# Optimization experiments

Hardware: AMD Instinct MI355X
Metric: run time of the kernel (lower is better)

Reference implementation:

```python
import jax, jax.numpy as jnp
import numpy as np

B, S, D = 4, 2048, 1024
H = 16
DH = D // H  # head dim = 64
LN_EPS = 1e-5


def setup_inputs() -> dict:
    key = jax.random.key(0)
    ks = jax.random.split(key, 4)
    scale = 1.0 / np.sqrt(D)
    return {
        "hidden_states": jax.random.normal(ks[0], (B, S, D), dtype=jnp.float32),
        "ln_gamma": jnp.ones((D,), jnp.float32),
        "ln_beta": jnp.zeros((D,), jnp.float32),
        "Wq": jax.random.normal(ks[1], (D, D), dtype=jnp.float32) * scale,
        "bq": jnp.zeros((D,), jnp.float32),
        "Wk": jax.random.normal(ks[2], (D, D), dtype=jnp.float32) * scale,
        "bk": jnp.zeros((D,), jnp.float32),
        "Wv": jax.random.normal(ks[3], (D, D), dtype=jnp.float32) * scale,
        "bv": jnp.zeros((D,), jnp.float32),
    }


def _layernorm(x, gamma, beta):
    mu = jnp.mean(x, axis=-1, keepdims=True)
    var = jnp.mean(jnp.square(x - mu), axis=-1, keepdims=True)
    return (x - mu) * jax.lax.rsqrt(var + LN_EPS) * gamma + beta


def reference(hidden_states, ln_gamma, ln_beta, Wq, bq, Wk, bk, Wv, bv):
    x = _layernorm(hidden_states, ln_gamma, ln_beta)  # [B,S,D]
    # Linear uses y = x @ W.T + b (torch convention)
    q = x @ Wq.T + bq
    k = x @ Wk.T + bk
    v = x @ Wv.T + bv
    # split heads -> [B,H,S,DH]
    q = q.reshape(B, S, H, DH).transpose(0, 2, 1, 3)
    k = k.reshape(B, S, H, DH).transpose(0, 2, 1, 3)
    v = v.reshape(B, S, H, DH).transpose(0, 2, 1, 3)
    scores = jnp.einsum("bhsd,bhtd->bhst", q, k) / jnp.sqrt(jnp.float32(DH))
    probs = jax.nn.softmax(scores, axis=-1)
    ctx = jnp.einsum("bhst,bhtd->bhsd", probs, v)  # [B,H,S,DH]
    ctx = ctx.transpose(0, 2, 1, 3).reshape(B, S, H * DH)
    return ctx
```

## Files before the change

kernel.cpp:

```cpp
#include <hip/hip_runtime.h>

#define B_ 4
#define S_ 2048
#define D_ 1024
#define H_ 16
#define DH_ 64
#define M_ (B_*S_)
#define N_ (3*D_)
#define K_ D_

using f32x4 = __attribute__((ext_vector_type(4))) float;
using s16x8 = __attribute__((ext_vector_type(8))) short;
typedef unsigned short u16;
typedef unsigned int u32;

__device__ __forceinline__ u16 f2bf(float f) {
  u32 u = __float_as_uint(f);
  return (u16)((u + 0x7FFFu + ((u >> 16) & 1u)) >> 16);
}

__device__ __forceinline__ u32 cvt_pk_bf16(float lo, float hi) {
  u32 r;
  asm("v_cvt_pk_bf16_f32 %0, %1, %2" : "=v"(r) : "v"(lo), "v"(hi));
  return r;
}

__device__ __forceinline__ float hw_exp2(float x) {
#if __has_builtin(__builtin_amdgcn_exp2f)
  return __builtin_amdgcn_exp2f(x);
#else
  return exp2f(x);
#endif
}

__device__ __forceinline__ void pswap32(u32& a, u32& b) {
#if __has_builtin(__builtin_amdgcn_permlane32_swap)
  auto r = __builtin_amdgcn_permlane32_swap(a, b, false, false);
  a = r[0]; b = r[1];
#else
  asm volatile("v_permlane32_swap_b32 %0, %1" : "+v"(a), "+v"(b));
#endif
}
__device__ __forceinline__ void pswap16(u32& a, u32& b) {
#if __has_builtin(__builtin_amdgcn_permlane16_swap)
  auto r = __builtin_amdgcn_permlane16_swap(a, b, false, false);
  a = r[0]; b = r[1];
#else
  asm volatile("v_permlane16_swap_b32 %0, %1" : "+v"(a), "+v"(b));
#endif
}

__device__ __forceinline__ void gload16(const void* g, void* l) {
  __builtin_amdgcn_global_load_lds((const __attribute__((address_space(1))) u32*)g,
                                   (__attribute__((address_space(3))) u32*)l,
                                   16, 0, 0);
}

__global__ __launch_bounds__(256) void k_lnw(const float* __restrict__ hs,
                                             const float* __restrict__ gam,
                                             const float* __restrict__ bet,
                                             const float* __restrict__ wq,
                                             const float* __restrict__ wk,
                                             const float* __restrict__ wv,
                                             u16* __restrict__ xln,
                                             u16* __restrict__ wcat) {
  __shared__ float ps[4], ps2[4];
  int tid = threadIdx.x;
  if (blockIdx.x < M_) {
    int row = blockIdx.x;
    const float4* src = (const float4*)(hs + (size_t)row * D_);
    float4 x = src[tid];
    float s = x.x + x.y + x.z + x.w;
    float s2 = x.x * x.x + x.y * x.y + x.z * x.z + x.w * x.w;
#pragma unroll
    for (int m = 32; m >= 1; m >>= 1) {
      s += __shfl_xor(s, m, 64);
      s2 += __shfl_xor(s2, m, 64);
    }
    int w = tid >> 6, lane = tid & 63;
    if (lane == 0) { ps[w] = s; ps2[w] = s2; }
    __syncthreads();
    s = ps[0] + ps[1] + ps[2] + ps[3];
    s2 = ps2[0] + ps2[1] + ps2[2] + ps2[3];
    float mean = s * (1.0f / D_);
    float var = s2 * (1.0f / D_) - mean * mean;
    float inv = 1.0f / sqrtf(var + 1e-5f);
    float4 g4 = ((const float4*)gam)[tid];
    float4 b4 = ((const float4*)bet)[tid];
    ushort4 o;
    o.x = f2bf((x.x - mean) * inv * g4.x + b4.x);
    o.y = f2bf((x.y - mean) * inv * g4.y + b4.y);
    o.z = f2bf((x.z - mean) * inv * g4.z + b4.z);
    o.w = f2bf((x.w - mean) * inv * g4.w + b4.w);
    *(ushort4*)(xln + (size_t)row * D_ + tid * 4) = o;
  } else {
    int idx = (blockIdx.x - M_) * 256 + tid;
    int seg = idx >> 18;
    int off = idx & 262143;
    const float* src = (seg == 0) ? wq : (seg == 1) ? wk : wv;
    float4 x = ((const float4*)src)[off];
    ushort4 o;
    o.x = f2bf(x.x); o.y = f2bf(x.y); o.z = f2bf(x.z); o.w = f2bf(x.w);
    ((ushort4*)wcat)[idx] = o;
  }
}

#define BM 256
#define BN 128
#define BK 64
__global__ __launch_bounds__(512, 4) void k_qkv(const u16* __restrict__ xln,
                                                const u16* __restrict__ wcat,
                                                const float* __restrict__ bq,
                                                const float* __restrict__ bk,
                                                const float* __restrict__ bv,
                                                u16* __restrict__ qh,
                                                u16* __restrict__ kh,
                                                u16* __restrict__ vt) {
  __shared__ char smem[49152];
  char* smA = smem;
  char* smB = smem + BM * BK * 2;
  int blk = (blockIdx.x & 7) * 96 + (blockIdx.x >> 3);
  int bm = blk / (N_ / BN);
  int bn = blk % (N_ / BN);
  int tid = threadIdx.x;
  int lane = tid & 63, wid = tid >> 6;
  int wm = wid >> 1, wn = wid & 1;
  int lo = lane & 15, hi = lane >> 4;
  int mBase = bm * BM, nBase = bn * BN;

  f32x4 acc[4][4];
  f32x4 zero = {0.f, 0.f, 0.f, 0.f};
#pragma unroll
  for (int i = 0; i < 4; ++i)
#pragma unroll
    for (int j = 0; j < 4; ++j) acc[i][j] = zero;

  for (int kt = 0; kt < K_ / BK; ++kt) {
#pragma unroll
    for (int i = 0; i < 4; ++i) {
      int id = i * 512 + tid;
      int r = id >> 3, c = id & 7;
      gload16(xln + (size_t)(mBase + r) * K_ + kt * BK + ((c ^ (r & 7)) << 3), smA + id * 16);
    }
#pragma unroll
    for (int i = 0; i < 2; ++i) {
      int id = i * 512 + tid;
      int r = id >> 3, c = id & 7;
      gload16(wcat + (size_t)(nBase + r) * K_ + kt * BK + ((c ^ (r & 7)) << 3), smB + id * 16);
    }
    asm volatile("s_waitcnt vmcnt(0)" ::: "memory");
    __syncthreads();
#pragma unroll
    for (int ks = 0; ks < 2; ++ks) {
      s16x8 a[4], b[4];
#pragma unroll
      for (int mi = 0; mi < 4; ++mi) {
        int r = wm * 64 + mi * 16 + lo;
        int cw = ks * 4 + hi;
        a[mi] = *(const s16x8*)(smA + r * 128 + ((cw ^ (r & 7)) << 4));
      }
#pragma unroll
      for (int ni = 0; ni < 4; ++ni) {
        int r = wn * 64 + ni * 16 + lo;
        int cw = ks * 4 + hi;
        b[ni] = *(const s16x8*)(smB + r * 128 + ((cw ^ (r & 7)) << 4));
      }
#pragma unroll
      for (int mi = 0; mi < 4; ++mi)
#pragma unroll
        for (int ni = 0; ni < 4; ++ni)
          acc[mi][ni] = __builtin_amdgcn_mfma_f32_16x16x32_bf16(a[mi], b[ni], acc[mi][ni], 0, 0, 0);
    }
    __syncthreads();
  }

  int mat = nBase >> 10;
  int bb = mBase >> 11;
  if (mat < 2) {
    const float* bias = (mat == 0) ? bq : bk;
    u16* dstb = (mat == 0) ? qh : kh;
    float scl = (mat == 0) ? 0.18033688011f : 1.0f;
#pragma unroll
    for (int mi = 0; mi < 4; ++mi)
#pragma unroll
      for (int ni = 0; ni < 4; ++ni)
#pragma unroll
        for (int r = 0; r < 4; ++r) {
          int m = mBase + wm * 64 + mi * 16 + hi * 4 + r;
          int n = nBase + wn * 64 + ni * 16 + lo;
          int o = n & 1023, h = o >> 6, dh = o & 63;
          float v = (acc[mi][ni][r] + bias[o]) * scl;
          dstb[((size_t)(bb * H_ + h) * S_ + (m & 2047)) * DH_ + dh] = f2bf(v);
        }
  } else {
    int tloc = mBase & 2047;
    __syncthreads();
#pragma unroll
    for (int p = 0; p < 2; ++p) {
      if ((wm >> 1) == p) {
        int mrow = (wm & 1) * 64;
#pragma unroll
        for (int mi = 0; mi < 4; ++mi)
#pragma unroll
          for (int ni = 0; ni < 4; ++ni) {
            int nl = wn * 64 + ni * 16 + lo;
            float bv_ = bv[(nBase + nl) & 1023];
#pragma unroll
            for (int r = 0; r < 4; ++r) {
              int ml = mrow + mi * 16 + hi * 4 + r;
              *(u16*)(smem + nl * 272 + ml * 2) = f2bf(acc[mi][ni][r] + bv_);
            }
          }
      }
      __syncthreads();
#pragma unroll
      for (int i = 0; i < 4; ++i) {
        int id = i * 512 + tid;
        int row = id >> 4, col = id & 15;
        uint4 x = *(const uint4*)(smem + row * 272 + col * 16);
        int o = (nBase + row) & 1023, h = o >> 6, dh = o & 63;
        *(uint4*)(vt + ((size_t)(bb * H_ + h) * DH_ + dh) * S_ + tloc + p * 128 + col * 8) = x;
      }
      __syncthreads();
    }
  }
}


#define QK_TILE(KB, da, db)                                                         \
    __builtin_amdgcn_s_setprio(1);                                                  \
    _Pragma("unroll")                                                               \
    for (int ft = 0; ft < 4; ++ft) {                                                \
      s16x8 kf = *(const s16x8*)(smem + (KB) + base0 + ft * 2048);                  \
      da[ft] = __builtin_amdgcn_mfma_f32_16x16x32_bf16(kf, qf00, minit, 0, 0, 0);   \
      db[ft] = __builtin_amdgcn_mfma_f32_16x16x32_bf16(kf, qf10, minit, 0, 0, 0);   \
    }                                                                               \
    _Pragma("unroll")                                                               \
    for (int ft = 0; ft < 4; ++ft) {                                                \
      s16x8 kf = *(const s16x8*)(smem + (KB) + base1 + ft * 2048);                  \
      da[ft] = __builtin_amdgcn_mfma_f32_16x16x32_bf16(kf, qf01, da[ft], 0, 0, 0);  \
      db[ft] = __builtin_amdgcn_mfma_f32_16x16x32_bf16(kf, qf11, db[ft], 0, 0, 0);  \
    }                                                                               \
    __builtin_amdgcn_s_setprio(0);

#define SM_PV(KB, da, db)                                                           \
  {                                                                                 \
    _Pragma("unroll")                                                               \
    for (int ft = 0; ft < 4; ++ft)                                                  \
      _Pragma("unroll")                                                             \
      for (int r = 0; r < 4; ++r) {                                                 \
        da[ft][r] = hw_exp2(da[ft][r]);                                             \
        db[ft][r] = hw_exp2(db[ft][r]);                                             \
      }                                                                             \
    union { u32 u[4]; s16x8 v; } pa0, pa1, pb0, pb1;                                \
    {                                                                               \
      u32 wz[8];                                                                    \
      _Pragma("unroll")                                                             \
      for (int ft = 0; ft < 4; ++ft) {                                              \
        wz[2 * ft]     = cvt_pk_bf16(da[ft][0], da[ft][1]);                         \
        wz[2 * ft + 1] = cvt_pk_bf16(da[ft][2], da[ft][3]);                         \
      }                                                                             \
      { u32 a = wz[0], b = wz[2]; pswap32(a, b); pswap16(a, b); pa0.u[0] = a; pa0.u[2] = b; } \
      { u32 a = wz[1], b = wz[3]; pswap32(a, b); pswap16(a, b); pa0.u[1] = a; pa0.u[3] = b; } \
      { u32 a = wz[4], b = wz[6]; pswap32(a, b); pswap16(a, b); pa1.u[0] = a; pa1.u[2] = b; } \
      { u32 a = wz[5], b = wz[7]; pswap32(a, b); pswap16(a, b); pa1.u[1] = a; pa1.u[3] = b; } \
    }                                                                               \
    {                                                                               \
      u32 wz[8];                                                                    \
      _Pragma("unroll")                                                             \
      for (int ft = 0; ft < 4; ++ft) {                                              \
        wz[2 * ft]     = cvt_pk_bf16(db[ft][0], db[ft][1]);                         \
        wz[2 * ft + 1] = cvt_pk_bf16(db[ft][2], db[ft][3]);                         \
      }                                                                             \
      { u32 a = wz[0], b = wz[2]; pswap32(a, b); pswap16(a, b); pb0.u[0] = a; pb0.u[2] = b; } \
      { u32 a = wz[1], b = wz[3]; pswap32(a, b); pswap16(a, b); pb0.u[1] = a; pb0.u[3] = b; } \
      { u32 a = wz[4], b = wz[6]; pswap32(a, b); pswap16(a, b); pb1.u[0] = a; pb1.u[2] = b; } \
      { u32 a = wz[5], b = wz[7]; pswap32(a, b); pswap16(a, b); pb1.u[1] = a; pb1.u[3] = b; } \
    }                                                                               \
    __builtin_amdgcn_s_setprio(1);                                                  \
    lacc0 = __builtin_amdgcn_mfma_f32_16x16x32_bf16(onesA.v, pa0.v, lacc0, 0, 0, 0);\
    lacc1 = __builtin_amdgcn_mfma_f32_16x16x32_bf16(onesA.v, pb0.v, lacc1, 0, 0, 0);\
    _Pragma("unroll")                                                               \
    for (int nf = 0; nf < 4; ++nf) {                                                \
      s16x8 vf = *(const s16x8*)(smem + 32768 + (KB) + base0 + nf * 2048);          \
      oacc0[nf] = __builtin_amdgcn_mfma_f32_16x16x32_bf16(vf, pa0.v, oacc0[nf], 0, 0, 0); \
      oacc1[nf] = __builtin_amdgcn_mfma_f32_16x16x32_bf16(vf, pb0.v, oacc1[nf], 0, 0, 0); \
    }                                                                               \
    lacc0 = __builtin_amdgcn_mfma_f32_16x16x32_bf16(onesA.v, pa1.v, lacc0, 0, 0, 0);\
    lacc1 = __builtin_amdgcn_mfma_f32_16x16x32_bf16(onesA.v, pb1.v, lacc1, 0, 0, 0);\
    _Pragma("unroll")                                                               \
    for (int nf = 0; nf < 4; ++nf) {                                                \
      s16x8 vf = *(const s16x8*)(smem + 32768 + (KB) + base1 + nf * 2048);          \
      oacc0[nf] = __builtin_amdgcn_mfma_f32_16x16x32_bf16(vf, pa1.v, oacc0[nf], 0, 0, 0); \
      oacc1[nf] = __builtin_amdgcn_mfma_f32_16x16x32_bf16(vf, pb1.v, oacc1[nf], 0, 0, 0); \
    }                                                                               \
    __builtin_amdgcn_s_setprio(0);                                                  \
  }

#define APERIOD(KB0, KB1, PKB0, PKB1, PF, WN)                                       \
  {                                                                                 \
    __builtin_amdgcn_s_barrier();                                                   \
    if (PF) {                                                                       \
      gload16(kpa, smem + (PKB0) + tid16);                                          \
      gload16(kpb, smem + (PKB0) + 4096 + tid16);                                   \
      gload16(vpa, smem + 32768 + (PKB0) + tid16);                                  \
      gload16(vpb, smem + 32768 + (PKB0) + 4096 + tid16);                           \
      kpa += 4096; kpb += 4096; vpa += 64; vpb += 64;                               \
      gload16(kpa, smem + (PKB1) + tid16);                                          \
      gload16(kpb, smem + (PKB1) + 4096 + tid16);                                   \
      gload16(vpa, smem + 32768 + (PKB1) + tid16);                                  \
      gload16(vpb, smem + 32768 + (PKB1) + 4096 + tid16);                           \
      kpa += 4096; kpb += 4096; vpa += 64; vpb += 64;                               \
    }                                                                               \
    asm volatile("s_waitcnt vmcnt(" #WN ")" ::: "memory");                          \
    f32x4 sa[4], sb[4], ua[4], ub[4];                                               \
    QK_TILE(KB0, sa, sb);                                                           \
    QK_TILE(KB1, ua, ub);                                                           \
    SM_PV(KB0, sa, sb);                                                             \
    SM_PV(KB1, ua, ub);                                                             \
  }

__global__ __launch_bounds__(256, 2) void k_attn(const u16* __restrict__ qh,
                                                 const u16* __restrict__ kh,
                                                 const u16* __restrict__ vt,
                                                 float* __restrict__ out) {
  __shared__ char smem[65536];
  int blk = (blockIdx.x & 7) * 128 + (blockIdx.x >> 3);
  int bh = blk >> 4, qt = blk & 15;
  int tid = threadIdx.x, lane = tid & 63, w = tid >> 6;
  int lo16 = lane & 15, hi = lane >> 4;
  int tid16 = tid * 16;

  const u16* qg = qh + (size_t)bh * S_ * DH_ + (size_t)qt * 128 * DH_;
  const u16* kg = kh + (size_t)bh * S_ * DH_;
  const u16* vg = vt + (size_t)bh * DH_ * S_;

  int r8 = tid >> 3, c8 = tid & 7;
  const u16* kpa = kg + r8 * 64 + ((c8 ^ (r8 & 7)) << 3);
  const u16* kpb = kpa + 2048;
  const u16* vpa = vg + r8 * 2048 + ((c8 ^ (r8 & 7)) << 3);
  const u16* vpb = vpa + 65536;

  const u16* qrow0 = qg + (size_t)(w * 32 + lo16) * 64 + hi * 8;
  const u16* qrow1 = qrow0 + 16 * 64;
  s16x8 qf00 = *(const s16x8*)(qrow0);
  s16x8 qf01 = *(const s16x8*)(qrow0 + 32);
  s16x8 qf10 = *(const s16x8*)(qrow1);
  s16x8 qf11 = *(const s16x8*)(qrow1 + 32);

#pragma unroll
  for (int p = 0; p < 2; ++p) {
    gload16(kpa, smem + p * 8192 + tid16);
    gload16(kpb, smem + p * 8192 + 4096 + tid16);
    gload16(vpa, smem + 32768 + p * 8192 + tid16);
    gload16(vpb, smem + 32768 + p * 8192 + 4096 + tid16);
    kpa += 4096; kpb += 4096; vpa += 64; vpb += 64;
  }

  int base0 = lo16 * 128 + ((hi ^ (lo16 & 7)) << 4);
  int base1 = lo16 * 128 + (((4 + hi) ^ (lo16 & 7)) << 4);

  f32x4 oacc0[4], oacc1[4], lacc0, lacc1;
  f32x4 zero = {0.f, 0.f, 0.f, 0.f};
#pragma unroll
  for (int nf = 0; nf < 4; ++nf) { oacc0[nf] = zero; oacc1[nf] = zero; }
  lacc0 = zero; lacc1 = zero;

  union { u32 u[4]; s16x8 v; } onesA;
#pragma unroll
  for (int j = 0; j < 4; ++j) onesA.u[j] = 0x3F803F80u;

  const f32x4 minit = {-16.f, -16.f, -16.f, -16.f};

  for (int pp = 0; pp < 7; ++pp) {
    APERIOD(0,     8192,  16384, 24576, true, 8);
    APERIOD(16384, 24576, 0,     8192,  true, 8);
  }
  APERIOD(0,     8192,  16384, 24576, true,  8);
  APERIOD(16384, 24576, 0,     0,     false, 0);

  float inv0 = 1.0f / lacc0[0];
  float inv1 = 1.0f / lacc1[0];
#pragma unroll
  for (int nf = 0; nf < 4; ++nf) { oacc0[nf] *= inv0; oacc1[nf] *= inv1; }

  __syncthreads();

  char* smO = smem + w * 8704;
#pragma unroll
  for (int nf = 0; nf < 4; ++nf) {
    *(f32x4*)(smO + lo16 * 272 + nf * 64 + hi * 16) = oacc0[nf];
    *(f32x4*)(smO + (16 + lo16) * 272 + nf * 64 + hi * 16) = oacc1[nf];
  }
  asm volatile("s_waitcnt lgkmcnt(0)" ::: "memory");

  int b = bh >> 4, h = bh & 15;
  int q2 = lane >> 2, part = lane & 3;
#pragma unroll
  for (int g = 0; g < 2; ++g) {
    int s_row = qt * 128 + w * 32 + g * 16 + q2;
    float* dst = out + ((size_t)(b * S_ + s_row)) * D_ + h * DH_;
#pragma unroll
    for (int c = 0; c < 4; ++c) {
      f32x4 v = *(const f32x4*)(smO + (g * 16 + q2) * 272 + c * 64 + part * 16);
      *(f32x4*)(dst + c * 16 + part * 4) = v;
    }
  }
}

extern "C" void kernel_launch(void* const* d_in, const int* in_sizes, int n_in,
                              void* d_out, int out_size, void* d_ws, size_t ws_size,
                              hipStream_t stream) {
  const float* hs = (const float*)d_in[0];
  const float* gam = (const float*)d_in[1];
  const float* bet = (const float*)d_in[2];
  const float* wq = (const float*)d_in[3];
  const float* bq = (const float*)d_in[4];
  const float* wk = (const float*)d_in[5];
  const float* bk = (const float*)d_in[6];
  const float* wv = (const float*)d_in[7];
  const float* bv = (const float*)d_in[8];
  float* outp = (float*)d_out;

  char* ws = (char*)d_ws;
  u16* xln  = (u16*)(ws);
  u16* wcat = (u16*)(ws + (16ull << 20));
  u16* qh   = (u16*)(ws + (24ull << 20));
  u16* kh   = (u16*)(ws + (40ull << 20));
  u16* vt   = (u16*)(ws + (56ull << 20));

  k_lnw<<<M_ + 3072, 256, 0, stream>>>(hs, gam, bet, wq, wk, wv, xln, wcat);
  k_qkv<<<(M_ / BM) * (N_ / BN), 512, 0, stream>>>(xln, wcat, bq, bk, bv, qh, kh, vt);
  k_attn<<<1024, 256, 0, stream>>>(qh, kh, vt, outp);
}
```

Baseline: 145.9 us.

## Double attention query tile to 256 rows per block with 64 rows per wave

The attention kernel now gives each block 256 query rows, each wave 64 rows as four 16-row groups, so every K and V tile loaded into shared memory serves twice as many queries. Grid size halves to 512 blocks, and the output epilogue stages through shared memory in two passes because the larger tile no longer fits at once. This cuts K/V global and LDS traffic per query, but raises register pressure from 16 score tiles and 16 output accumulators, which may cause spills under the 2-blocks-per-CU launch bound. Fewer blocks also leave less parallelism to fill the GPU.

```diff
diff --git a/kernel.cpp b/kernel.cpp
--- a/kernel.cpp
+++ b/kernel.cpp
@@ -227,72 +227,66 @@
 }
 
 
-#define QK_TILE(KB, da, db)                                                         \
+#define ATILE4(KB)                                                                  \
+  {                                                                                 \
+    f32x4 st[4][4];                                                                 \
     __builtin_amdgcn_s_setprio(1);                                                  \
     _Pragma("unroll")                                                               \
     for (int ft = 0; ft < 4; ++ft) {                                                \
       s16x8 kf = *(const s16x8*)(smem + (KB) + base0 + ft * 2048);                  \
-      da[ft] = __builtin_amdgcn_mfma_f32_16x16x32_bf16(kf, qf00, minit, 0, 0, 0);   \
-      db[ft] = __builtin_amdgcn_mfma_f32_16x16x32_bf16(kf, qf10, minit, 0, 0, 0);   \
+      _Pragma("unroll")                                                             \
+      for (int g = 0; g < 4; ++g)                                                   \
+        st[g][ft] = __builtin_amdgcn_mfma_f32_16x16x32_bf16(kf, qf0[g], minit, 0, 0, 0); \
     }                                                                               \
     _Pragma("unroll")                                                               \
     for (int ft = 0; ft < 4; ++ft) {                                                \
       s16x8 kf = *(const s16x8*)(smem + (KB) + base1 + ft * 2048);                  \
-      da[ft] = __builtin_amdgcn_mfma_f32_16x16x32_bf16(kf, qf01, da[ft], 0, 0, 0);  \
-      db[ft] = __builtin_amdgcn_mfma_f32_16x16x32_bf16(kf, qf11, db[ft], 0, 0, 0);  \
-    }                                                                               \
-    __builtin_amdgcn_s_setprio(0);
-
-#define SM_PV(KB, da, db)                                                           \
-  {                                                                                 \
-    _Pragma("unroll")                                                               \
-    for (int ft = 0; ft < 4; ++ft)                                                  \
-      _Pragma("unroll")                                                             \
-      for (int r = 0; r < 4; ++r) {                                                 \
-        da[ft][r] = hw_exp2(da[ft][r]);                                             \
-        db[ft][r] = hw_exp2(db[ft][r]);                                             \
+      _Pragma("unroll")                                                             \
+      for (int g = 0; g < 4; ++g)                                                   \
+        st[g][ft] = __builtin_amdgcn_mfma_f32_16x16x32_bf16(kf, qf1[g], st[g][ft], 0, 0, 0); \
+    }                                                                               \
+    __builtin_amdgcn_s_setprio(0);                                                  \
+    _Pragma("unroll")                                                               \
+    for (int g = 0; g < 4; ++g)                                                     \
+      _Pragma("unroll")                                                             \
+      for (int ft = 0; ft < 4; ++ft)                                                \
+        _Pragma("unroll")                                                           \
+        for (int r = 0; r < 4; ++r)                                                 \
+          st[g][ft][r] = hw_exp2(st[g][ft][r]);                                     \
+    union { u32 u[4]; s16x8 v; } pf0[4], pf1[4];                                    \
+    _Pragma("unroll")                                                               \
+    for (int g = 0; g < 4; ++g) {                                                   \
+      u32 wz[8];                                                                    \
+      _Pragma("unroll")                                                             \
+      for (int ft = 0; ft < 4; ++ft) {                                              \
+        wz[2 * ft]     = cvt_pk_bf16(st[g][ft][0], st[g][ft][1]);                   \
+        wz[2 * ft + 1] = cvt_pk_bf16(st[g][ft][2], st[g][ft][3]);                   \
       }                                                                             \
-    union { u32 u[4]; s16x8 v; } pa0, pa1, pb0, pb1;                                \
-    {                                                                               \
-      u32 wz[8];                                                                    \
-      _Pragma("unroll")                                                             \
-      for (int ft = 0; ft < 4; ++ft) {                                              \
-        wz[2 * ft]     = cvt_pk_bf16(da[ft][0], da[ft][1]);                         \
-        wz[2 * ft + 1] = cvt_pk_bf16(da[ft][2], da[ft][3]);                         \
-      }                                                                             \
-      { u32 a = wz[0], b = wz[2]; pswap32(a, b); pswap16(a, b); pa0.u[0] = a; pa0.u[2] = b; } \
-      { u32 a = wz[1], b = wz[3]; pswap32(a, b); pswap16(a, b); pa0.u[1] = a; pa0.u[3] = b; } \
-      { u32 a = wz[4], b = wz[6]; pswap32(a, b); pswap16(a, b); pa1.u[0] = a; pa1.u[2] = b; } \
-      { u32 a = wz[5], b = wz[7]; pswap32(a, b); pswap16(a, b); pa1.u[1] = a; pa1.u[3] = b; } \
-    }                                                                               \
-    {                                                                               \
-      u32 wz[8];                                                                    \
-      _Pragma("unroll")                                                             \
-      for (int ft = 0; ft < 4; ++ft) {                                              \
-        wz[2 * ft]     = cvt_pk_bf16(db[ft][0], db[ft][1]);                         \
-        wz[2 * ft + 1] = cvt_pk_bf16(db[ft][2], db[ft][3]);                         \
-      }                                                                             \
-      { u32 a = wz[0], b = wz[2]; pswap32(a, b); pswap16(a, b); pb0.u[0] = a; pb0.u[2] = b; } \
-      { u32 a = wz[1], b = wz[3]; pswap32(a, b); pswap16(a, b); pb0.u[1] = a; pb0.u[3] = b; } \
-      { u32 a = wz[4], b = wz[6]; pswap32(a, b); pswap16(a, b); pb1.u[0] = a; pb1.u[2] = b; } \
-      { u32 a = wz[5], b = wz[7]; pswap32(a, b); pswap16(a, b); pb1.u[1] = a; pb1.u[3] = b; } \
+      { u32 a = wz[0], b = wz[2]; pswap32(a, b); pswap16(a, b); pf0[g].u[0] = a; pf0[g].u[2] = b; } \
+      { u32 a = wz[1], b = wz[3]; pswap32(a, b); pswap16(a, b); pf0[g].u[1] = a; pf0[g].u[3] = b; } \
+      { u32 a = wz[4], b = wz[6]; pswap32(a, b); pswap16(a, b); pf1[g].u[0] = a; pf1[g].u[2] = b; } \
+      { u32 a = wz[5], b = wz[7]; pswap32(a, b); pswap16(a, b); pf1[g].u[1] = a; pf1[g].u[3] = b; } \
     }                                                                               \
     __builtin_amdgcn_s_setprio(1);                                                  \
-    lacc0 = __builtin_amdgcn_mfma_f32_16x16x32_bf16(onesA.v, pa0.v, lacc0, 0, 0, 0);\
-    lacc1 = __builtin_amdgcn_mfma_f32_16x16x32_bf16(onesA.v, pb0.v, lacc1, 0, 0, 0);\
+    _Pragma("unroll")                                                               \
+    for (int g = 0; g < 4; ++g)                                                     \
+      lacc[g] = __builtin_amdgcn_mfma_f32_16x16x32_bf16(onesA.v, pf0[g].v, lacc[g], 0, 0, 0); \
     _Pragma("unroll")                                                               \
     for (int nf = 0; nf < 4; ++nf) {                                                \
       s16x8 vf = *(const s16x8*)(smem + 32768 + (KB) + base0 + nf * 2048);          \
-      oacc0[nf] = __builtin_amdgcn_mfma_f32_16x16x32_bf16(vf, pa0.v, oacc0[nf], 0, 0, 0); \
-      oacc1[nf] = __builtin_amdgcn_mfma_f32_16x16x32_bf16(vf, pb0.v, oacc1[nf], 0, 0, 0); \
-    }                                                                               \
-    lacc0 = __builtin_amdgcn_mfma_f32_16x16x32_bf16(onesA.v, pa1.v, lacc0, 0, 0, 0);\
-    lacc1 = __builtin_amdgcn_mfma_f32_16x16x32_bf16(onesA.v, pb1.v, lacc1, 0, 0, 0);\
+      _Pragma("unroll")                                                             \
+      for (int g = 0; g < 4; ++g)                                                   \
+        oacc[g][nf] = __builtin_amdgcn_mfma_f32_16x16x32_bf16(vf, pf0[g].v, oacc[g][nf], 0, 0, 0); \
+    }                                                                               \
+    _Pragma("unroll")                                                               \
+    for (int g = 0; g < 4; ++g)                                                     \
+      lacc[g] = __builtin_amdgcn_mfma_f32_16x16x32_bf16(onesA.v, pf1[g].v, lacc[g], 0, 0, 0); \
     _Pragma("unroll")                                                               \
     for (int nf = 0; nf < 4; ++nf) {                                                \
       s16x8 vf = *(const s16x8*)(smem + 32768 + (KB) + base1 + nf * 2048);          \
-      oacc0[nf] = __builtin_amdgcn_mfma_f32_16x16x32_bf16(vf, pa1.v, oacc0[nf], 0, 0, 0); \
-      oacc1[nf] = __builtin_amdgcn_mfma_f32_16x16x32_bf16(vf, pb1.v, oacc1[nf], 0, 0, 0); \
+      _Pragma("unroll")                                                             \
+      for (int g = 0; g < 4; ++g)                                                   \
+        oacc[g][nf] = __builtin_amdgcn_mfma_f32_16x16x32_bf16(vf, pf1[g].v, oacc[g][nf], 0, 0, 0); \
     }                                                                               \
     __builtin_amdgcn_s_setprio(0);                                                  \
   }
@@ -313,11 +307,8 @@
       kpa += 4096; kpb += 4096; vpa += 64; vpb += 64;                               \
     }                                                                               \
     asm volatile("s_waitcnt vmcnt(" #WN ")" ::: "memory");                          \
-    f32x4 sa[4], sb[4], ua[4], ub[4];                                               \
-    QK_TILE(KB0, sa, sb);                                                           \
-    QK_TILE(KB1, ua, ub);                                                           \
-    SM_PV(KB0, sa, sb);                                                             \
-    SM_PV(KB1, ua, ub);                                                             \
+    ATILE4(KB0);                                                                    \
+    ATILE4(KB1);                                                                    \
   }
 
 __global__ __launch_bounds__(256, 2) void k_attn(const u16* __restrict__ qh,
@@ -325,13 +316,13 @@
                                                  const u16* __restrict__ vt,
                                                  float* __restrict__ out) {
   __shared__ char smem[65536];
-  int blk = (blockIdx.x & 7) * 128 + (blockIdx.x >> 3);
-  int bh = blk >> 4, qt = blk & 15;
+  int blk = (blockIdx.x & 7) * 64 + (blockIdx.x >> 3);
+  int bh = blk >> 3, qt = blk & 7;
   int tid = threadIdx.x, lane = tid & 63, w = tid >> 6;
   int lo16 = lane & 15, hi = lane >> 4;
   int tid16 = tid * 16;
 
-  const u16* qg = qh + (size_t)bh * S_ * DH_ + (size_t)qt * 128 * DH_;
+  const u16* qg = qh + (size_t)bh * S_ * DH_ + (size_t)qt * 256 * DH_;
   const u16* kg = kh + (size_t)bh * S_ * DH_;
   const u16* vg = vt + (size_t)bh * DH_ * S_;
 
@@ -341,12 +332,13 @@
   const u16* vpa = vg + r8 * 2048 + ((c8 ^ (r8 & 7)) << 3);
   const u16* vpb = vpa + 65536;
 
-  const u16* qrow0 = qg + (size_t)(w * 32 + lo16) * 64 + hi * 8;
-  const u16* qrow1 = qrow0 + 16 * 64;
-  s16x8 qf00 = *(const s16x8*)(qrow0);
-  s16x8 qf01 = *(const s16x8*)(qrow0 + 32);
-  s16x8 qf10 = *(const s16x8*)(qrow1);
-  s16x8 qf11 = *(const s16x8*)(qrow1 + 32);
+  s16x8 qf0[4], qf1[4];
+#pragma unroll
+  for (int g = 0; g < 4; ++g) {
+    const u16* qrow = qg + (size_t)(w * 64 + g * 16 + lo16) * 64 + hi * 8;
+    qf0[g] = *(const s16x8*)(qrow);
+    qf1[g] = *(const s16x8*)(qrow + 32);
+  }
 
 #pragma unroll
   for (int p = 0; p < 2; ++p) {
@@ -360,11 +352,14 @@
   int base0 = lo16 * 128 + ((hi ^ (lo16 & 7)) << 4);
   int base1 = lo16 * 128 + (((4 + hi) ^ (lo16 & 7)) << 4);
 
-  f32x4 oacc0[4], oacc1[4], lacc0, lacc1;
+  f32x4 oacc[4][4], lacc[4];
   f32x4 zero = {0.f, 0.f, 0.f, 0.f};
 #pragma unroll
-  for (int nf = 0; nf < 4; ++nf) { oacc0[nf] = zero; oacc1[nf] = zero; }
-  lacc0 = zero; lacc1 = zero;
+  for (int g = 0; g < 4; ++g) {
+    lacc[g] = zero;
+#pragma unroll
+    for (int nf = 0; nf < 4; ++nf) oacc[g][nf] = zero;
+  }
 
   union { u32 u[4]; s16x8 v; } onesA;
 #pragma unroll
@@ -379,32 +374,39 @@
   APERIOD(0,     8192,  16384, 24576, true,  8);
   APERIOD(16384, 24576, 0,     0,     false, 0);
 
-  float inv0 = 1.0f / lacc0[0];
-  float inv1 = 1.0f / lacc1[0];
-#pragma unroll
-  for (int nf = 0; nf < 4; ++nf) { oacc0[nf] *= inv0; oacc1[nf] *= inv1; }
-
-  __syncthreads();
-
-  char* smO = smem + w * 8704;
-#pragma unroll
-  for (int nf = 0; nf < 4; ++nf) {
-    *(f32x4*)(smO + lo16 * 272 + nf * 64 + hi * 16) = oacc0[nf];
-    *(f32x4*)(smO + (16 + lo16) * 272 + nf * 64 + hi * 16) = oacc1[nf];
-  }
-  asm volatile("s_waitcnt lgkmcnt(0)" ::: "memory");
+#pragma unroll
+  for (int g = 0; g < 4; ++g) {
+    float inv = 1.0f / lacc[g][0];
+#pragma unroll
+    for (int nf = 0; nf < 4; ++nf) oacc[g][nf] *= inv;
+  }
 
   int b = bh >> 4, h = bh & 15;
   int q2 = lane >> 2, part = lane & 3;
-#pragma unroll
-  for (int g = 0; g < 2; ++g) {
-    int s_row = qt * 128 + w * 32 + g * 16 + q2;
-    float* dst = out + ((size_t)(b * S_ + s_row)) * D_ + h * DH_;
-#pragma unroll
-    for (int c = 0; c < 4; ++c) {
-      f32x4 v = *(const f32x4*)(smO + (g * 16 + q2) * 272 + c * 64 + part * 16);
-      *(f32x4*)(dst + c * 16 + part * 4) = v;
-    }
+
+  __syncthreads();
+#pragma unroll
+  for (int pass = 0; pass < 2; ++pass) {
+    if ((w >> 1) == pass) {
+      char* smO = smem + (w & 1) * 17408;
+#pragma unroll
+      for (int g = 0; g < 4; ++g)
+#pragma unroll
+        for (int nf = 0; nf < 4; ++nf)
+          *(f32x4*)(smO + (g * 16 + lo16) * 272 + nf * 64 + hi * 16) = oacc[g][nf];
+      asm volatile("s_waitcnt lgkmcnt(0)" ::: "memory");
+#pragma unroll
+      for (int g = 0; g < 4; ++g) {
+        int s_row = qt * 256 + w * 64 + g * 16 + q2;
+        float* dst = out + ((size_t)(b * S_ + s_row)) * D_ + h * DH_;
+#pragma unroll
+        for (int c = 0; c < 4; ++c) {
+          f32x4 v = *(const f32x4*)(smO + (g * 16 + q2) * 272 + c * 64 + part * 16);
+          *(f32x4*)(dst + c * 16 + part * 4) = v;
+        }
+      }
+    }
+    __syncthreads();
   }
 }
 
@@ -431,5 +433,5 @@
 
   k_lnw<<<M_ + 3072, 256, 0, stream>>>(hs, gam, bet, wq, wk, wv, xln, wcat);
   k_qkv<<<(M_ / BM) * (N_ / BN), 512, 0, stream>>>(xln, wcat, bq, bk, bv, qh, kh, vt);
-  k_attn<<<1024, 256, 0, stream>>>(qh, kh, vt, outp);
-}
+  k_attn<<<512, 256, 0, stream>>>(qh, kh, vt, outp);
+}
```

Measured after the change: 141.7 us, median of 3. -2.9%, faster.
